# Optimization experiments

Measured on AMD Instinct MI355X. Metric: run time of the kernel, lower is better.

## Reference

```python
import jax, jax.numpy as jnp
import numpy as np

N_EXP, N_DICT, N_PIX = 2048, 65536, 1600

def setup_inputs() -> dict:
    key = jax.random.key(0)
    k1, k2, k3 = jax.random.split(key, 3)
    return {
        "experimental_data": jax.random.normal(k1, (N_EXP, N_PIX), dtype=jnp.float32),
        "patterns": jax.random.normal(k2, (N_DICT, N_PIX), dtype=jnp.float32),
        "so3_samples_fz": jax.random.normal(k3, (N_DICT, 4), dtype=jnp.float32),
        "topk": 10,
    }

def reference(experimental_data, patterns, so3_samples_fz, topk):
    # di_patterns: subtract per-pattern mean from experimental data
    q = experimental_data - jnp.mean(experimental_data, axis=1, keepdims=True)
    # _project_dictionary: dictionary patterns are mean-subtracted at projection time
    d = patterns - jnp.mean(patterns, axis=1, keepdims=True)
    # angular distance metric: normalize, dot, arccos; min angle == max cosine
    qn = q * jax.lax.rsqrt(jnp.sum(q * q, axis=1, keepdims=True))
    dn = d * jax.lax.rsqrt(jnp.sum(d * d, axis=1, keepdims=True))
    cos_sim = jnp.einsum("qp,dp->qd", qn, dn)            # [n_exp, n_dict]
    top_cos, top_idx = jax.lax.top_k(cos_sim, topk)       # [n_exp, topk]
    top_ang = jnp.arccos(jnp.clip(top_cos, -1.0, 1.0))    # angular distance of matches
    # lookup_orientations: gather matched quaternions from the SO(3) FZ sampling
    orientations = so3_samples_fz[top_idx]                # [n_exp, topk, 4]
    return top_ang, top_idx, orientations
```

## Files before the change

kernel.cpp:

```cpp
#include <hip/hip_runtime.h>
#include <stdint.h>

#define N_EXP  2048
#define N_DICT 65536
#define N_PIX  1600
#define TOPK   10
#define K1     16
#define KTH    8
#define K2     16
#define NBLK   512
#define NCAND  (NBLK * 4)

#define BM 128
#define BN 128
#define BK 64
#define KTILES (N_PIX / BK)

typedef __attribute__((ext_vector_type(8))) __bf16 bf16x8;
typedef __attribute__((ext_vector_type(4))) float  f32x4;

__device__ __forceinline__ unsigned short f2bf(float f) {
    unsigned int u = __float_as_uint(f);
    unsigned int r = (u + 0x7FFFu + ((u >> 16) & 1u)) >> 16;
    return (unsigned short)r;
}

__device__ __forceinline__ float sel4f(const float a[4], int p) {
    return p == 0 ? a[0] : (p == 1 ? a[1] : (p == 2 ? a[2] : a[3]));
}
__device__ __forceinline__ int sel4i(const int a[4], int p) {
    return p == 0 ? a[0] : (p == 1 ? a[1] : (p == 2 ? a[2] : a[3]));
}

__device__ __forceinline__ float blockReduceSumF(float v) {
    __shared__ float p[4];
    #pragma unroll
    for (int o = 32; o > 0; o >>= 1) v += __shfl_down(v, o);
    __syncthreads();
    if ((threadIdx.x & 63) == 0) p[threadIdx.x >> 6] = v;
    __syncthreads();
    return p[0] + p[1] + p[2] + p[3];
}

__global__ __launch_bounds__(256) void prep_rows(const float* __restrict__ in,
                                                 unsigned short* __restrict__ outb) {
    const int row = blockIdx.x;
    const int tid = threadIdx.x;
    const float* x = in + (size_t)row * N_PIX;
    float v[7];
    float s = 0.f;
    #pragma unroll
    for (int it = 0; it < 7; ++it) {
        int j = tid + it * 256;
        float t = (j < N_PIX) ? x[j] : 0.f;
        v[it] = t; s += t;
    }
    s = blockReduceSumF(s);
    const float mean = s * (1.0f / N_PIX);
    float ss = 0.f;
    #pragma unroll
    for (int it = 0; it < 7; ++it) {
        int j = tid + it * 256;
        float c = v[it] - mean;
        if (j < N_PIX) ss += c * c;
    }
    ss = blockReduceSumF(ss);
    const float rn = rsqrtf(ss);
    unsigned short* o = outb + (size_t)row * N_PIX;
    #pragma unroll
    for (int it = 0; it < 7; ++it) {
        int j = tid + it * 256;
        if (j < N_PIX) o[j] = f2bf((v[it] - mean) * rn);
    }
}

__global__ __launch_bounds__(256) void gemm_topk(const unsigned short* __restrict__ A,
                                                 const unsigned short* __restrict__ B,
                                                 float* __restrict__ cand_s,
                                                 int* __restrict__ cand_i) {
    __shared__ __attribute__((aligned(16))) char smem[32768];
    unsigned short* As = (unsigned short*)smem;
    unsigned short* Bs = (unsigned short*)(smem + 16384);
    float*          Ss = (float*)smem;

    const int tid  = threadIdx.x;
    const int lane = tid & 63;
    const int w    = tid >> 6;
    const int wm   = w >> 1, wn = w & 1;

    const int id  = blockIdx.x;
    const int xcd = id & 7;
    const int j_  = id >> 3;
    const int bm  = j_ & 15;
    const int bn  = (j_ >> 4) * 8 + xcd;

    const unsigned short* Ag = A + (size_t)bm * BM * N_PIX;
    const unsigned short* Bg = B + (size_t)bn * BN * N_PIX;

    const int ldr = lane >> 3;
    const int ldc = (((lane & 7) ^ ldr) * 8);
    const int m    = lane & 15;
    const int quad = lane >> 4;

    f32x4 acc[4][4];
    #pragma unroll
    for (int i = 0; i < 4; ++i)
        #pragma unroll
        for (int j = 0; j < 4; ++j)
            acc[i][j] = (f32x4){0.f, 0.f, 0.f, 0.f};

    for (int kt = 0; kt < KTILES; ++kt) {
        const int k0 = kt * BK;
        #pragma unroll
        for (int t = 0; t < 4; ++t) {
            int r = w * 32 + t * 8 + ldr;
            __builtin_amdgcn_global_load_lds(
                (const __attribute__((address_space(1))) void*)(const void*)(Ag + (size_t)r * N_PIX + k0 + ldc),
                (__attribute__((address_space(3))) void*)(void*)((char*)As + (w * 4 + t) * 1024),
                16, 0, 0);
            __builtin_amdgcn_global_load_lds(
                (const __attribute__((address_space(1))) void*)(const void*)(Bg + (size_t)r * N_PIX + k0 + ldc),
                (__attribute__((address_space(3))) void*)(void*)((char*)Bs + (w * 4 + t) * 1024),
                16, 0, 0);
        }
        __syncthreads();
        #pragma unroll
        for (int ks = 0; ks < BK; ks += 32) {
            bf16x8 af[4], bfr[4];
            const int kc = (ks >> 3) + quad;
            const int sw = (kc ^ (m & 7)) * 8;
            #pragma unroll
            for (int i = 0; i < 4; ++i)
                af[i] = *(const bf16x8*)(&As[(wm * 64 + i * 16 + m) * BK + sw]);
            #pragma unroll
            for (int j = 0; j < 4; ++j)
                bfr[j] = *(const bf16x8*)(&Bs[(wn * 64 + j * 16 + m) * BK + sw]);
            #pragma unroll
            for (int i = 0; i < 4; ++i)
                #pragma unroll
                for (int j = 0; j < 4; ++j)
                    acc[i][j] = __builtin_amdgcn_mfma_f32_16x16x32_bf16(af[i], bfr[j], acc[i][j], 0, 0, 0);
        }
        __syncthreads();
    }

    const int row4 = tid >> 2;
    const int part = tid & 3;

    #pragma unroll
    for (int half = 0; half < 2; ++half) {
        __syncthreads();
        if (wm == half) {
            #pragma unroll
            for (int i = 0; i < 4; ++i)
                #pragma unroll
                for (int r = 0; r < 4; ++r) {
                    int row = i * 16 + quad * 4 + r;
                    #pragma unroll
                    for (int j = 0; j < 4; ++j) {
                        int col = wn * 64 + j * 16 + m;
                        Ss[row * 128 + ((col + row) & 127)] = acc[i][j][r];
                    }
                }
        }
        __syncthreads();
        float bs4[4]; int bi4[4];
        bs4[0] = bs4[1] = bs4[2] = bs4[3] = -2.0f;
        bi4[0] = bi4[1] = bi4[2] = bi4[3] = 0;
        #pragma unroll
        for (int k = 0; k < 32; ++k) {
            int col = part * 32 + ((k + 8 * part) & 31);
            float v = Ss[row4 * 128 + ((col + row4) & 127)];
            if (v > bs4[3]) {
                int cix = bn * 128 + col;
                #pragma unroll
                for (int t = 0; t < 4; ++t) {
                    bool sw = v > bs4[t];
                    float ts = bs4[t]; int ti = bi4[t];
                    bs4[t] = sw ? v : ts;  bi4[t] = sw ? cix : ti;
                    v = sw ? ts : v;       cix = sw ? ti : cix;
                }
            }
        }
        #pragma unroll
        for (int s = 1; s <= 2; s <<= 1) {
            float ov[4]; int oi[4];
            #pragma unroll
            for (int t = 0; t < 4; ++t) {
                ov[t] = __shfl_xor(bs4[t], s);
                oi[t] = __shfl_xor(bi4[t], s);
            }
            float rv[4]; int ri[4]; int pa = 0, pb = 0;
            #pragma unroll
            for (int t = 0; t < 4; ++t) {
                float va = sel4f(bs4, pa), vb = sel4f(ov, pb);
                bool ta = (va >= vb);
                rv[t] = ta ? va : vb;
                ri[t] = ta ? sel4i(bi4, pa) : sel4i(oi, pb);
                pa += ta ? 1 : 0; pb += ta ? 0 : 1;
            }
            #pragma unroll
            for (int t = 0; t < 4; ++t) { bs4[t] = rv[t]; bi4[t] = ri[t]; }
        }
        if (part == 0) {
            int grow = bm * BM + half * 64 + row4;
            *(float4*)(cand_s + (size_t)grow * NCAND + bn * 4) =
                make_float4(bs4[0], bs4[1], bs4[2], bs4[3]);
            *(int4*)(cand_i + (size_t)grow * NCAND + bn * 4) =
                make_int4(bi4[0], bi4[1], bi4[2], bi4[3]);
        }
    }
}

__global__ __launch_bounds__(256) void merge_cands(const float* __restrict__ cand_s,
                                                   const int* __restrict__ cand_i,
                                                   int* __restrict__ sel_g) {
    __shared__ float Ms[256 * K1];
    __shared__ int   Mi[256 * K1];
    const int row = blockIdx.x, tid = threadIdx.x;
    const float* s = cand_s + (size_t)row * NCAND;
    const int*   x = cand_i + (size_t)row * NCAND;

    float ls[KTH]; int li[KTH];
    #pragma unroll
    for (int t = 0; t < KTH; ++t) { ls[t] = -2.f; li[t] = 0; }
    #pragma unroll
    for (int it = 0; it < NCAND / 256; ++it) {
        int j = tid + it * 256;
        float v = s[j];
        if (v > ls[KTH - 1]) {
            float cv = v; int ci = x[j];
            #pragma unroll
            for (int t = 0; t < KTH; ++t) {
                bool sw = cv > ls[t];
                float ts = ls[t]; int ti = li[t];
                ls[t] = sw ? cv : ts; li[t] = sw ? ci : ti;
                cv = sw ? ts : cv;   ci = sw ? ti : ci;
            }
        }
    }
    #pragma unroll
    for (int t = 0; t < KTH; ++t) { Ms[tid * K1 + t] = ls[t]; Mi[tid * K1 + t] = li[t]; }
    #pragma unroll
    for (int t = KTH; t < K1; ++t) { Ms[tid * K1 + t] = -3.f; Mi[tid * K1 + t] = 0; }
    __syncthreads();

    #pragma unroll
    for (int lev = 0; lev < 8; ++lev) {
        int stride = 1 << lev;
        if ((tid & (2 * stride - 1)) == 0) {
            int ia = tid * K1, ib = (tid + stride) * K1;
            float rs[K1]; int ri[K1];
            int pa = 0, pb = 0;
            #pragma unroll
            for (int t = 0; t < K1; ++t) {
                float va = Ms[ia + pa], vb = Ms[ib + pb];
                bool ta = (va >= vb);
                rs[t] = ta ? va : vb;
                ri[t] = ta ? Mi[ia + pa] : Mi[ib + pb];
                pa += ta ? 1 : 0; pb += ta ? 0 : 1;
            }
            #pragma unroll
            for (int t = 0; t < K1; ++t) { Ms[ia + t] = rs[t]; Mi[ia + t] = ri[t]; }
        }
        __syncthreads();
    }
    if (tid < K1) sel_g[(size_t)row * K1 + tid] = Mi[tid];
}

__global__ __launch_bounds__(256) void refine_out(const float* __restrict__ expd,
                                                  const float* __restrict__ pat,
                                                  const float* __restrict__ so3,
                                                  const int* __restrict__ sel_g,
                                                  float* __restrict__ out) {
    __shared__ double qc[N_PIX];
    __shared__ double pd[4], pd2[4], pd3[4];
    __shared__ int    sel[K2];
    __shared__ double cosv[K2];
    const int row = blockIdx.x, tid = threadIdx.x;
    const float* x = expd + (size_t)row * N_PIX;

    double s1 = 0.0;
    for (int j = tid; j < N_PIX; j += 256) s1 += (double)x[j];
    #pragma unroll
    for (int o = 32; o > 0; o >>= 1) s1 += __shfl_down(s1, o);
    if ((tid & 63) == 0) pd[tid >> 6] = s1;
    __syncthreads();
    const double mean = (pd[0] + pd[1] + pd[2] + pd[3]) * (1.0 / N_PIX);

    double s2 = 0.0, sc = 0.0;
    for (int j = tid; j < N_PIX; j += 256) {
        double c = (double)x[j] - mean;
        qc[j] = c; s2 += c * c; sc += c;
    }
    #pragma unroll
    for (int o = 32; o > 0; o >>= 1) { s2 += __shfl_down(s2, o); sc += __shfl_down(sc, o); }
    if ((tid & 63) == 0) { pd2[tid >> 6] = s2; pd3[tid >> 6] = sc; }
    if (tid < K2) sel[tid] = sel_g[(size_t)row * K2 + tid];
    __syncthreads();
    const double sumsq = pd2[0] + pd2[1] + pd2[2] + pd2[3];
    const double sqc   = pd3[0] + pd3[1] + pd3[2] + pd3[3];
    const double invq  = 1.0 / sqrt(sumsq);

    const int c  = tid >> 4;
    const int sl = tid & 15;
    const int di = sel[c];
    const float* p = pat + (size_t)di * N_PIX;
    double sp = 0.0, spp = 0.0, sqp = 0.0;
    for (int j = sl; j < N_PIX; j += 16) {
        double pv = (double)p[j];
        sp += pv; spp += pv * pv; sqp += qc[j] * pv;
    }
    #pragma unroll
    for (int o = 8; o > 0; o >>= 1) {
        sp  += __shfl_down(sp,  o, 16);
        spp += __shfl_down(spp, o, 16);
        sqp += __shfl_down(sqp, o, 16);
    }
    if (sl == 0) {
        double mp   = sp * (1.0 / N_PIX);
        double varp = spp - sp * sp * (1.0 / N_PIX);
        double invd = 1.0 / sqrt(varp);
        cosv[c] = (sqp - mp * sqc) * invq * invd;
    }
    __syncthreads();

    if (tid == 0) {
        double cv[K2]; int ci[K2];
        for (int t = 0; t < K2; ++t) { cv[t] = cosv[t]; ci[t] = sel[t]; }
        for (int a = 1; a < K2; ++a) {
            double kv = cv[a]; int ki = ci[a];
            int b = a - 1;
            while (b >= 0 && (cv[b] < kv || (cv[b] == kv && ci[b] > ki))) {
                cv[b + 1] = cv[b]; ci[b + 1] = ci[b]; --b;
            }
            cv[b + 1] = kv; ci[b + 1] = ki;
        }
        float* oa = out;
        float* oi = out + (size_t)N_EXP * TOPK;
        float* oo = out + (size_t)2 * N_EXP * TOPK;
        for (int r = 0; r < TOPK; ++r) {
            double cc = cv[r];
            if (cc > 1.0) cc = 1.0;
            if (cc < -1.0) cc = -1.0;
            oa[(size_t)row * TOPK + r] = (float)acos(cc);
            oi[(size_t)row * TOPK + r] = (float)ci[r];
            int q4 = ci[r];
            #pragma unroll
            for (int t = 0; t < 4; ++t)
                oo[((size_t)row * TOPK + r) * 4 + t] = so3[(size_t)q4 * 4 + t];
        }
    }
}

extern "C" void kernel_launch(void* const* d_in, const int* in_sizes, int n_in,
                              void* d_out, int out_size, void* d_ws, size_t ws_size,
                              hipStream_t stream) {
    const float* expd = (const float*)d_in[0];
    const float* pat  = (const float*)d_in[1];
    const float* so3  = (const float*)d_in[2];
    float* out = (float*)d_out;
    char* ws = (char*)d_ws;

    const size_t QB = (size_t)N_EXP  * N_PIX * 2;
    const size_t DB = (size_t)N_DICT * N_PIX * 2;
    const size_t CB = (size_t)N_EXP  * NCAND * 4;

    unsigned short* Qb = (unsigned short*)ws;
    unsigned short* Db = (unsigned short*)(ws + QB);
    float* cs  = (float*)(ws + QB + DB);
    int*   ci  = (int*)  (ws + QB + DB + CB);
    int*   sel = (int*)  (ws + QB + DB + 2 * CB);

    prep_rows<<<N_EXP, 256, 0, stream>>>(expd, Qb);
    prep_rows<<<N_DICT, 256, 0, stream>>>(pat, Db);
    gemm_topk<<<(N_EXP / BM) * (N_DICT / BN), 256, 0, stream>>>(Qb, Db, cs, ci);
    merge_cands<<<N_EXP, 256, 0, stream>>>(cs, ci, sel);
    refine_out<<<N_EXP, 256, 0, stream>>>(expd, pat, so3, sel, out);
}
```

Measured before the change: 1.491 ms.

## Double-buffer 256x256 GEMM tiles with async LDS prefetch and wider per-tile top-k

The similarity GEMM grows from 128x128 tiles on 256 threads to 256x256 tiles on 512 threads, with 128KB of dynamic LDS. It also adds a software pipeline: two LDS buffers are filled by global_load_lds while MFMAs run on the other buffer. Phases are split by fine-grained vmcnt waits and barriers, and MFMA sections run at raised priority. The goal is to hide global-load latency and raise arithmetic intensity per byte loaded. Each tile now keeps 8 candidates per row instead of 4, so the candidate buffer keeps the same size, at the cost of a heavier insertion sort and merge in the epilogue.

```diff
diff --git a/kernel.cpp b/kernel.cpp
--- a/kernel.cpp
+++ b/kernel.cpp
@@ -8,13 +8,13 @@
 #define K1     16
 #define KTH    8
 #define K2     16
-#define NBLK   512
-#define NCAND  (NBLK * 4)
-
-#define BM 128
-#define BN 128
+#define NBLK   256
+#define NCAND  (NBLK * 8)
+
+#define BM 256
+#define BN 256
 #define BK 64
-#define KTILES (N_PIX / BK)
+#define KT 25
 
 typedef __attribute__((ext_vector_type(8))) __bf16 bf16x8;
 typedef __attribute__((ext_vector_type(4))) float  f32x4;
@@ -25,11 +25,17 @@
     return (unsigned short)r;
 }
 
-__device__ __forceinline__ float sel4f(const float a[4], int p) {
-    return p == 0 ? a[0] : (p == 1 ? a[1] : (p == 2 ? a[2] : a[3]));
-}
-__device__ __forceinline__ int sel4i(const int a[4], int p) {
-    return p == 0 ? a[0] : (p == 1 ? a[1] : (p == 2 ? a[2] : a[3]));
+__device__ __forceinline__ float sel8f(const float a[8], int p) {
+    float r = a[0];
+    #pragma unroll
+    for (int t = 1; t < 8; ++t) r = (p == t) ? a[t] : r;
+    return r;
+}
+__device__ __forceinline__ int sel8i(const int a[8], int p) {
+    int r = a[0];
+    #pragma unroll
+    for (int t = 1; t < 8; ++t) r = (p == t) ? a[t] : r;
+    return r;
 }
 
 __device__ __forceinline__ float blockReduceSumF(float v) {
@@ -74,76 +80,118 @@
     }
 }
 
-__global__ __launch_bounds__(256) void gemm_topk(const unsigned short* __restrict__ A,
-                                                 const unsigned short* __restrict__ B,
-                                                 float* __restrict__ cand_s,
-                                                 int* __restrict__ cand_i) {
-    __shared__ __attribute__((aligned(16))) char smem[32768];
-    unsigned short* As = (unsigned short*)smem;
-    unsigned short* Bs = (unsigned short*)(smem + 16384);
-    float*          Ss = (float*)smem;
+__device__ __forceinline__ void glds16(const unsigned short* g, char* l) {
+    __builtin_amdgcn_global_load_lds(
+        (const __attribute__((address_space(1))) void*)(const void*)g,
+        (__attribute__((address_space(3))) void*)(void*)l, 16, 0, 0);
+}
+
+#define BAR() do { asm volatile("" ::: "memory"); \
+                   __builtin_amdgcn_s_barrier(); \
+                   __builtin_amdgcn_sched_barrier(0); } while (0)
+
+__global__ __launch_bounds__(512, 2) void gemm_topk(const unsigned short* __restrict__ A,
+                                                    const unsigned short* __restrict__ B,
+                                                    float* __restrict__ cand_s,
+                                                    int* __restrict__ cand_i) {
+    extern __shared__ char smem[];
 
     const int tid  = threadIdx.x;
     const int lane = tid & 63;
     const int w    = tid >> 6;
-    const int wm   = w >> 1, wn = w & 1;
+    const int wm   = w >> 2;
+    const int wn   = w & 3;
+    const int m    = lane & 15;
+    const int quad = lane >> 4;
 
     const int id  = blockIdx.x;
     const int xcd = id & 7;
     const int j_  = id >> 3;
-    const int bm  = j_ & 15;
-    const int bn  = (j_ >> 4) * 8 + xcd;
+    const int bm  = j_ & 7;
+    const int bn  = (j_ >> 3) * 8 + xcd;
 
     const unsigned short* Ag = A + (size_t)bm * BM * N_PIX;
     const unsigned short* Bg = B + (size_t)bn * BN * N_PIX;
 
-    const int ldr = lane >> 3;
-    const int ldc = (((lane & 7) ^ ldr) * 8);
-    const int m    = lane & 15;
-    const int quad = lane >> 4;
-
-    f32x4 acc[4][4];
-    #pragma unroll
-    for (int i = 0; i < 4; ++i)
+    const int srow = w * 16 + (lane >> 2);
+    const int scol = ((lane & 3) ^ ((lane >> 3) & 3)) * 8;
+    const unsigned short* sA = Ag + (size_t)srow * N_PIX + scol;
+    const unsigned short* sB = Bg + (size_t)srow * N_PIX + scol;
+    char* dst0 = smem + w * 1024;
+
+    const int chunk = (quad ^ ((m >> 1) & 3)) * 16;
+    const int aoff  = (wm * 128 + m) * 64 + chunk;
+    const int boff  = 32768 + (wn * 64 + m) * 64 + chunk;
+
+    f32x4 acc[8][4];
+    #pragma unroll
+    for (int i = 0; i < 8; ++i)
         #pragma unroll
         for (int j = 0; j < 4; ++j)
             acc[i][j] = (f32x4){0.f, 0.f, 0.f, 0.f};
 
-    for (int kt = 0; kt < KTILES; ++kt) {
-        const int k0 = kt * BK;
-        #pragma unroll
-        for (int t = 0; t < 4; ++t) {
-            int r = w * 32 + t * 8 + ldr;
-            __builtin_amdgcn_global_load_lds(
-                (const __attribute__((address_space(1))) void*)(const void*)(Ag + (size_t)r * N_PIX + k0 + ldc),
-                (__attribute__((address_space(3))) void*)(void*)((char*)As + (w * 4 + t) * 1024),
-                16, 0, 0);
-            __builtin_amdgcn_global_load_lds(
-                (const __attribute__((address_space(1))) void*)(const void*)(Bg + (size_t)r * N_PIX + k0 + ldc),
-                (__attribute__((address_space(3))) void*)(void*)((char*)Bs + (w * 4 + t) * 1024),
-                16, 0, 0);
-        }
-        __syncthreads();
-        #pragma unroll
-        for (int ks = 0; ks < BK; ks += 32) {
-            bf16x8 af[4], bfr[4];
-            const int kc = (ks >> 3) + quad;
-            const int sw = (kc ^ (m & 7)) * 8;
-            #pragma unroll
-            for (int i = 0; i < 4; ++i)
-                af[i] = *(const bf16x8*)(&As[(wm * 64 + i * 16 + m) * BK + sw]);
-            #pragma unroll
-            for (int j = 0; j < 4; ++j)
-                bfr[j] = *(const bf16x8*)(&Bs[(wn * 64 + j * 16 + m) * BK + sw]);
-            #pragma unroll
-            for (int i = 0; i < 4; ++i)
-                #pragma unroll
-                for (int j = 0; j < 4; ++j)
-                    acc[i][j] = __builtin_amdgcn_mfma_f32_16x16x32_bf16(af[i], bfr[j], acc[i][j], 0, 0, 0);
-        }
-        __syncthreads();
-    }
-
+    bf16x8 af[8];
+    bf16x8 bf2[2];
+
+#define STAGE(MAT, P, H, T) do {                                              \
+    const unsigned short* _s = ((MAT) ? sB : sA) + (T) * 64 + (H) * 32;       \
+    char* _d = dst0 + (P) * 65536 + (MAT) * 32768 + (H) * 16384;              \
+    glds16(_s, _d);                                                           \
+    glds16(_s + 128 * N_PIX, _d + 8192);                                      \
+} while (0)
+
+#define PHASE(P, KS, JH, DO, SM, SH, ST, VM) do {                                           \
+    if ((JH) == 0) {                                                                        \
+        _Pragma("unroll")                                                                   \
+        for (int i_ = 0; i_ < 8; ++i_)                                                      \
+            af[i_] = *(const bf16x8*)(smem + (P)*65536 + (KS)*16384 + i_*1024 + aoff);      \
+    }                                                                                       \
+    bf2[0] = *(const bf16x8*)(smem + (P)*65536 + (KS)*16384 + ((JH)*2+0)*1024 + boff);      \
+    bf2[1] = *(const bf16x8*)(smem + (P)*65536 + (KS)*16384 + ((JH)*2+1)*1024 + boff);      \
+    if (DO) STAGE(SM, (P)^1, SH, ST);                                                       \
+    if ((VM) == 4) asm volatile("s_waitcnt vmcnt(4)" ::: "memory");                         \
+    if ((VM) == 0) asm volatile("s_waitcnt vmcnt(0)" ::: "memory");                         \
+    BAR();                                                                                  \
+    __builtin_amdgcn_s_setprio(1);                                                          \
+    _Pragma("unroll")                                                                       \
+    for (int i_ = 0; i_ < 8; ++i_) {                                                        \
+        acc[i_][(JH)*2+0] = __builtin_amdgcn_mfma_f32_16x16x32_bf16(af[i_], bf2[0],         \
+                                                       acc[i_][(JH)*2+0], 0, 0, 0);         \
+        acc[i_][(JH)*2+1] = __builtin_amdgcn_mfma_f32_16x16x32_bf16(af[i_], bf2[1],         \
+                                                       acc[i_][(JH)*2+1], 0, 0, 0);         \
+    }                                                                                       \
+    __builtin_amdgcn_s_setprio(0);                                                          \
+    BAR();                                                                                  \
+} while (0)
+
+    STAGE(0, 0, 0, 0);
+    STAGE(1, 0, 0, 0);
+    STAGE(0, 0, 1, 0);
+    STAGE(1, 0, 1, 0);
+    asm volatile("s_waitcnt vmcnt(4)" ::: "memory");
+    BAR();
+
+    #pragma unroll 1
+    for (int t2 = 0; t2 < 12; ++t2) {
+        const int t0 = 2 * t2;
+        PHASE(0, 0, 0, 1, 0, 0, t0 + 1, -1);
+        PHASE(0, 0, 1, 1, 1, 0, t0 + 1,  4);
+        PHASE(0, 1, 0, 1, 0, 1, t0 + 1, -1);
+        PHASE(0, 1, 1, 1, 1, 1, t0 + 1,  4);
+        PHASE(1, 0, 0, 1, 0, 0, t0 + 2, -1);
+        PHASE(1, 0, 1, 1, 1, 0, t0 + 2,  4);
+        PHASE(1, 1, 0, 1, 0, 1, t0 + 2, -1);
+        PHASE(1, 1, 1, 1, 1, 1, t0 + 2,  4);
+    }
+    PHASE(0, 0, 0, 0, 0, 0, 0, -1);
+    PHASE(0, 0, 1, 0, 0, 0, 0,  0);
+    PHASE(0, 1, 0, 0, 0, 0, 0, -1);
+    PHASE(0, 1, 1, 0, 0, 0, 0, -1);
+
+#undef PHASE
+#undef STAGE
+
+    float* Ss = (float*)smem;
     const int row4 = tid >> 2;
     const int part = tid & 3;
 
@@ -152,62 +200,63 @@
         __syncthreads();
         if (wm == half) {
             #pragma unroll
-            for (int i = 0; i < 4; ++i)
+            for (int i = 0; i < 8; ++i)
                 #pragma unroll
                 for (int r = 0; r < 4; ++r) {
                     int row = i * 16 + quad * 4 + r;
                     #pragma unroll
                     for (int j = 0; j < 4; ++j) {
                         int col = wn * 64 + j * 16 + m;
-                        Ss[row * 128 + ((col + row) & 127)] = acc[i][j][r];
+                        Ss[row * 256 + ((col + row) & 255)] = acc[i][j][r];
                     }
                 }
         }
         __syncthreads();
-        float bs4[4]; int bi4[4];
-        bs4[0] = bs4[1] = bs4[2] = bs4[3] = -2.0f;
-        bi4[0] = bi4[1] = bi4[2] = bi4[3] = 0;
+        float bs[8]; int bi[8];
         #pragma unroll
-        for (int k = 0; k < 32; ++k) {
-            int col = part * 32 + ((k + 8 * part) & 31);
-            float v = Ss[row4 * 128 + ((col + row4) & 127)];
-            if (v > bs4[3]) {
-                int cix = bn * 128 + col;
+        for (int t = 0; t < 8; ++t) { bs[t] = -2.0f; bi[t] = 0; }
+        #pragma unroll
+        for (int k = 0; k < 64; ++k) {
+            int col = part * 64 + ((k + 16 * part) & 63);
+            float v = Ss[row4 * 256 + ((col + row4) & 255)];
+            if (v > bs[7]) {
+                int cix = bn * 256 + col;
                 #pragma unroll
-                for (int t = 0; t < 4; ++t) {
-                    bool sw = v > bs4[t];
-                    float ts = bs4[t]; int ti = bi4[t];
-                    bs4[t] = sw ? v : ts;  bi4[t] = sw ? cix : ti;
-                    v = sw ? ts : v;       cix = sw ? ti : cix;
+                for (int t = 0; t < 8; ++t) {
+                    bool sw = v > bs[t];
+                    float ts = bs[t]; int ti = bi[t];
+                    bs[t] = sw ? v : ts;  bi[t] = sw ? cix : ti;
+                    v = sw ? ts : v;      cix = sw ? ti : cix;
                 }
             }
         }
         #pragma unroll
         for (int s = 1; s <= 2; s <<= 1) {
-            float ov[4]; int oi[4];
-            #pragma unroll
-            for (int t = 0; t < 4; ++t) {
-                ov[t] = __shfl_xor(bs4[t], s);
-                oi[t] = __shfl_xor(bi4[t], s);
-            }
-            float rv[4]; int ri[4]; int pa = 0, pb = 0;
-            #pragma unroll
-            for (int t = 0; t < 4; ++t) {
-                float va = sel4f(bs4, pa), vb = sel4f(ov, pb);
+            float ov[8]; int oi[8];
+            #pragma unroll
+            for (int t = 0; t < 8; ++t) {
+                ov[t] = __shfl_xor(bs[t], s);
+                oi[t] = __shfl_xor(bi[t], s);
+            }
+            float rv[8]; int ri[8]; int pa = 0, pb = 0;
+            #pragma unroll
+            for (int t = 0; t < 8; ++t) {
+                float va = sel8f(bs, pa), vb = sel8f(ov, pb);
                 bool ta = (va >= vb);
                 rv[t] = ta ? va : vb;
-                ri[t] = ta ? sel4i(bi4, pa) : sel4i(oi, pb);
+                ri[t] = ta ? sel8i(bi, pa) : sel8i(oi, pb);
                 pa += ta ? 1 : 0; pb += ta ? 0 : 1;
             }
             #pragma unroll
-            for (int t = 0; t < 4; ++t) { bs4[t] = rv[t]; bi4[t] = ri[t]; }
+            for (int t = 0; t < 8; ++t) { bs[t] = rv[t]; bi[t] = ri[t]; }
         }
         if (part == 0) {
-            int grow = bm * BM + half * 64 + row4;
-            *(float4*)(cand_s + (size_t)grow * NCAND + bn * 4) =
-                make_float4(bs4[0], bs4[1], bs4[2], bs4[3]);
-            *(int4*)(cand_i + (size_t)grow * NCAND + bn * 4) =
-                make_int4(bi4[0], bi4[1], bi4[2], bi4[3]);
+            int grow = bm * BM + half * 128 + row4;
+            size_t base = (size_t)grow * NCAND + bn * 8;
+            *(float4*)(cand_s + base)     = make_float4(bs[0], bs[1], bs[2], bs[3]);
+            *(float4*)(cand_s + base + 4) = make_float4(bs[4], bs[5], bs[6], bs[7]);
+            *(int4*)(cand_i + base)       = make_int4(bi[0], bi[1], bi[2], bi[3]);
+            *(int4*)(cand_i + base + 4)   = make_int4(bi[4], bi[5], bi[6], bi[7]);
         }
     }
 }
@@ -362,6 +411,13 @@
     float* out = (float*)d_out;
     char* ws = (char*)d_ws;
 
+    static bool attr_set = false;
+    if (!attr_set) {
+        (void)hipFuncSetAttribute((const void*)gemm_topk,
+                                  hipFuncAttributeMaxDynamicSharedMemorySize, 131072);
+        attr_set = true;
+    }
+
     const size_t QB = (size_t)N_EXP  * N_PIX * 2;
     const size_t DB = (size_t)N_DICT * N_PIX * 2;
     const size_t CB = (size_t)N_EXP  * NCAND * 4;
@@ -374,7 +430,7 @@
 
     prep_rows<<<N_EXP, 256, 0, stream>>>(expd, Qb);
     prep_rows<<<N_DICT, 256, 0, stream>>>(pat, Db);
-    gemm_topk<<<(N_EXP / BM) * (N_DICT / BN), 256, 0, stream>>>(Qb, Db, cs, ci);
+    gemm_topk<<<(N_EXP / BM) * (N_DICT / BN), 512, 131072, stream>>>(Qb, Db, cs, ci);
     merge_cands<<<N_EXP, 256, 0, stream>>>(cs, ci, sel);
     refine_out<<<N_EXP, 256, 0, stream>>>(expd, pat, so3, sel, out);
 }
```

Measured after the change: 2.096 ms. +40.6%, slower.

## Double-buffer LDS tiles in GEMM to overlap global loads with MFMA

Applied to the files above, without the earlier changes.

The GEMM main loop now holds two 32KB LDS stages. It issues the direct-to-LDS loads for tile k+1 before computing on tile k, and waits with a partial vmcnt so the fetch overlaps the MFMA work. The LDS footprint doubles to 64KB per block, which may reduce occupancy, and raw barriers with sched_barrier replace __syncthreads.

```diff
diff --git a/kernel.cpp b/kernel.cpp
--- a/kernel.cpp
+++ b/kernel.cpp
@@ -74,14 +74,22 @@
     }
 }
 
+__device__ __forceinline__ void glds16(const unsigned short* g, char* l) {
+    __builtin_amdgcn_global_load_lds(
+        (const __attribute__((address_space(1))) void*)(const void*)g,
+        (__attribute__((address_space(3))) void*)(void*)l, 16, 0, 0);
+}
+
+#define BAR() do { asm volatile("" ::: "memory"); \
+                   __builtin_amdgcn_s_barrier(); \
+                   __builtin_amdgcn_sched_barrier(0); } while (0)
+
 __global__ __launch_bounds__(256) void gemm_topk(const unsigned short* __restrict__ A,
                                                  const unsigned short* __restrict__ B,
                                                  float* __restrict__ cand_s,
                                                  int* __restrict__ cand_i) {
-    __shared__ __attribute__((aligned(16))) char smem[32768];
-    unsigned short* As = (unsigned short*)smem;
-    unsigned short* Bs = (unsigned short*)(smem + 16384);
-    float*          Ss = (float*)smem;
+    __shared__ __attribute__((aligned(16))) char smem[65536];
+    float* Ss = (float*)smem;
 
     const int tid  = threadIdx.x;
     const int lane = tid & 63;
@@ -109,21 +117,32 @@
         for (int j = 0; j < 4; ++j)
             acc[i][j] = (f32x4){0.f, 0.f, 0.f, 0.f};
 
+#define STAGE_TILE(P, T) do {                                                     \
+    const int _k0 = (T) * BK;                                                     \
+    _Pragma("unroll")                                                             \
+    for (int t_ = 0; t_ < 4; ++t_) {                                              \
+        int r_ = w * 32 + t_ * 8 + ldr;                                           \
+        glds16(Ag + (size_t)r_ * N_PIX + _k0 + ldc,                               \
+               smem + (P) * 32768 + (w * 4 + t_) * 1024);                         \
+        glds16(Bg + (size_t)r_ * N_PIX + _k0 + ldc,                               \
+               smem + (P) * 32768 + 16384 + (w * 4 + t_) * 1024);                 \
+    }                                                                             \
+} while (0)
+
+    STAGE_TILE(0, 0);
+
+    #pragma unroll 1
     for (int kt = 0; kt < KTILES; ++kt) {
-        const int k0 = kt * BK;
-        #pragma unroll
-        for (int t = 0; t < 4; ++t) {
-            int r = w * 32 + t * 8 + ldr;
-            __builtin_amdgcn_global_load_lds(
-                (const __attribute__((address_space(1))) void*)(const void*)(Ag + (size_t)r * N_PIX + k0 + ldc),
-                (__attribute__((address_space(3))) void*)(void*)((char*)As + (w * 4 + t) * 1024),
-                16, 0, 0);
-            __builtin_amdgcn_global_load_lds(
-                (const __attribute__((address_space(1))) void*)(const void*)(Bg + (size_t)r * N_PIX + k0 + ldc),
-                (__attribute__((address_space(3))) void*)(void*)((char*)Bs + (w * 4 + t) * 1024),
-                16, 0, 0);
-        }
-        __syncthreads();
+        const int p = kt & 1;
+        if (kt + 1 < KTILES) {
+            STAGE_TILE(p ^ 1, kt + 1);
+            asm volatile("s_waitcnt vmcnt(8)" ::: "memory");
+        } else {
+            asm volatile("s_waitcnt vmcnt(0)" ::: "memory");
+        }
+        BAR();
+        const unsigned short* As = (const unsigned short*)(smem + p * 32768);
+        const unsigned short* Bs = (const unsigned short*)(smem + p * 32768 + 16384);
         #pragma unroll
         for (int ks = 0; ks < BK; ks += 32) {
             bf16x8 af[4], bfr[4];
@@ -141,8 +160,9 @@
                 for (int j = 0; j < 4; ++j)
                     acc[i][j] = __builtin_amdgcn_mfma_f32_16x16x32_bf16(af[i], bfr[j], acc[i][j], 0, 0, 0);
         }
-        __syncthreads();
-    }
+        BAR();
+    }
+#undef STAGE_TILE
 
     const int row4 = tid >> 2;
     const int part = tid & 3;
```

Measured after the change: 1.278 ms. 1.17x faster.
